# Kernel tuning notes

Hardware: AMD Instinct MI355X
Metric: run time of the kernel (lower is better)

Reference implementation:

```python
import jax, jax.numpy as jnp
import numpy as np

N_NODES = 100000
N_EDGES = 1600000
EPS = 1e-5


def _xavier(key, shape):
    fan_out, fan_in = shape
    lim = float(np.sqrt(6.0 / (fan_in + fan_out)))
    return jax.random.uniform(key, shape, jnp.float32, -lim, lim)


def setup_inputs() -> dict:
    key = jax.random.key(0)
    ks = jax.random.split(key, 16)
    d_in, d1, d2, d3 = 32, 64, 128, 64
    inp = {
        "x": jax.random.normal(ks[0], (N_NODES, d_in), jnp.float32),
        "edge_index": jax.random.randint(ks[1], (2, N_EDGES), 0, N_NODES, jnp.int64),
        "edge_weight": jax.random.uniform(ks[2], (N_EDGES,), jnp.float32),
        # GraphConv params: lin_rel (with bias) applied to aggregated msgs, lin_root (no bias)
        "W1_rel": _xavier(ks[3], (d1, d_in)), "b1": jnp.zeros((d1,), jnp.float32), "W1_root": _xavier(ks[4], (d1, d_in)),
        "W2_rel": _xavier(ks[5], (d2, d1)), "b2": jnp.zeros((d2,), jnp.float32), "W2_root": _xavier(ks[6], (d2, d1)),
        "W3_rel": _xavier(ks[7], (d3, d2)), "b3": jnp.zeros((d3,), jnp.float32), "W3_root": _xavier(ks[8], (d3, d2)),
        # BatchNorm affine params
        "g1": jnp.ones((d1,), jnp.float32), "be1": jnp.zeros((d1,), jnp.float32),
        "g2": jnp.ones((d2,), jnp.float32), "be2": jnp.zeros((d2,), jnp.float32),
        "g3": jnp.ones((d3,), jnp.float32), "be3": jnp.zeros((d3,), jnp.float32),
        # node-level classifier: Linear(64,32) -> ReLU -> Linear(32,2)
        "Wc1": _xavier(ks[9], (32, d3)), "bc1": jnp.zeros((32,), jnp.float32),
        "Wc2": _xavier(ks[10], (2, 32)), "bc2": jnp.zeros((2,), jnp.float32),
    }
    return inp


def _graph_conv(x, src, dst, W_rel, b, W_root, ew=None):
    msg = x[src]                      # [E, d] gather
    if ew is not None:
        msg = msg * ew[:, None]
    agg = jax.ops.segment_sum(msg, dst, num_segments=N_NODES)  # [N, d] scatter-add
    return agg @ W_rel.T + b + x @ W_root.T


def _bn(h, g, beta):
    mu = jnp.mean(h, axis=0)
    var = jnp.var(h, axis=0)
    return (h - mu) * jax.lax.rsqrt(var + EPS) * g + beta


def reference(x, edge_index, edge_weight,
              W1_rel, b1, W1_root, W2_rel, b2, W2_root, W3_rel, b3, W3_root,
              g1, be1, g2, be2, g3, be3, Wc1, bc1, Wc2, bc2):
    src, dst = edge_index[0], edge_index[1]
    h1 = jax.nn.relu(_bn(_graph_conv(x, src, dst, W1_rel, b1, W1_root), g1, be1))
    h2 = jax.nn.relu(_bn(_graph_conv(h1, src, dst, W2_rel, b2, W2_root), g2, be2))
    h3 = _bn(_graph_conv(h2, src, dst, W3_rel, b3, W3_root, edge_weight), g3, be3)
    h3 = jax.nn.relu(h3 + h1)  # residual (dims match, no projection)
    logits = jax.nn.relu(h3 @ Wc1.T + bc1) @ Wc2.T + bc2  # [N, 2]
    return logits
```

## Files before the change

### kernel.cpp

```cpp
#include <hip/hip_runtime.h>

#define N_NODES 100000
#define N_EDGES 1600000
#define EPSV 1e-5f

__device__ __forceinline__ ushort f2bf(float f) {
  unsigned u = __float_as_uint(f);
  unsigned r = (u + 0x7FFFu + ((u >> 16) & 1u)) >> 16;
  return (ushort)r;
}


__global__ void hist_kernel(const int* __restrict__ ei, int* __restrict__ cnt) {
  int e = blockIdx.x * blockDim.x + threadIdx.x;
  if (e >= N_EDGES) return;
  atomicAdd(&cnt[ei[N_EDGES + e]], 1);
}

#define SCAN_BLK 1024
#define SCAN_NB ((N_NODES + SCAN_BLK - 1) / SCAN_BLK)

__global__ void scan_phase1(const int* __restrict__ cnt, int* __restrict__ blocksum) {
  __shared__ int part[256];
  int base = blockIdx.x * SCAN_BLK + threadIdx.x * 4;
  int s = 0;
#pragma unroll
  for (int i = 0; i < 4; ++i) {
    int idx = base + i;
    if (idx < N_NODES) s += cnt[idx];
  }
  part[threadIdx.x] = s;
  __syncthreads();
  for (int d = 128; d > 0; d >>= 1) {
    if (threadIdx.x < d) part[threadIdx.x] += part[threadIdx.x + d];
    __syncthreads();
  }
  if (threadIdx.x == 0) blocksum[blockIdx.x] = part[0];
}

__global__ void scan_phase2(int* __restrict__ blocksum, int* __restrict__ rowptr) {
  __shared__ int part[128];
  int tid = threadIdx.x;
  int v = (tid < SCAN_NB) ? blocksum[tid] : 0;
  part[tid] = v;
  __syncthreads();
  for (int d = 1; d < 128; d <<= 1) {
    int t = (tid >= d) ? part[tid - d] : 0;
    __syncthreads();
    part[tid] += t;
    __syncthreads();
  }
  if (tid < SCAN_NB) blocksum[tid] = part[tid] - v;
  if (tid == 127) rowptr[N_NODES] = part[127];
}

__global__ void scan_phase3(const int* __restrict__ cnt, const int* __restrict__ blocksum,
                            int* __restrict__ rowptr, int* __restrict__ cursor) {
  __shared__ int part[256];
  int base = blockIdx.x * SCAN_BLK + threadIdx.x * 4;
  int c[4];
  int s = 0;
#pragma unroll
  for (int i = 0; i < 4; ++i) {
    int idx = base + i;
    c[i] = (idx < N_NODES) ? cnt[idx] : 0;
    s += c[i];
  }
  part[threadIdx.x] = s;
  __syncthreads();
  int me = s;
  for (int d = 1; d < 256; d <<= 1) {
    int t = (threadIdx.x >= d) ? part[threadIdx.x - d] : 0;
    __syncthreads();
    part[threadIdx.x] += t;
    __syncthreads();
  }
  int off = blocksum[blockIdx.x] + part[threadIdx.x] - me;
#pragma unroll
  for (int i = 0; i < 4; ++i) {
    int idx = base + i;
    if (idx < N_NODES) {
      rowptr[idx] = off;
      cursor[idx] = off;
      off += c[i];
    }
  }
}

#define FILL_SUB 256

__global__ void fill_kernel(const int* __restrict__ ei, const float* __restrict__ ew,
                            int* __restrict__ cursor, unsigned* __restrict__ col) {
  const int g = blockIdx.x & 7;
  const int sub = blockIdx.x >> 3;
  const int lo = g * 12500;
  const int hi = lo + 12500;
  const int EPB = (N_EDGES + FILL_SUB - 1) / FILL_SUB;
  const int beg = sub * EPB;
  const int end = min(beg + EPB, N_EDGES);
  for (int e = beg + (int)threadIdx.x; e < end; e += (int)blockDim.x) {
    int d = ei[N_EDGES + e];
    if (d < lo || d >= hi) continue;
    int p = atomicAdd(&cursor[d], 1);
    col[p] = ((unsigned)f2bf(ew[e]) << 17) | (unsigned)ei[e];
  }
}


__global__ void cast_bf16(const float* __restrict__ in, ushort* __restrict__ out, int n4) {
  int i = blockIdx.x * blockDim.x + threadIdx.x;
  if (i >= n4) return;
  float4 v = reinterpret_cast<const float4*>(in)[i];
  ushort4 o = make_ushort4(f2bf(v.x), f2bf(v.y), f2bf(v.z), f2bf(v.w));
  reinterpret_cast<ushort4*>(out)[i] = o;
}


#define SRC_OF(v) ((v) & 0x1FFFFu)
#define W_OF(v) __uint_as_float(((v) >> 17) << 16)

__global__ void gather_d32_bf(const ushort* __restrict__ xb, const int* __restrict__ rowptr,
                              const unsigned* __restrict__ col, float* __restrict__ agg) {
  int gid = blockIdx.x * blockDim.x + threadIdx.x;
  int n = gid >> 2;
  if (n >= N_NODES) return;
  int c = gid & 3;
  int beg = rowptr[n], end = rowptr[n + 1];
  float acc[8];
#pragma unroll
  for (int i = 0; i < 8; ++i) acc[i] = 0.f;
  int p = beg;
  for (; p + 1 < end; p += 2) {
    unsigned e0 = col[p], e1 = col[p + 1];
    uint4 u0 = *reinterpret_cast<const uint4*>(xb + (size_t)SRC_OF(e0) * 32 + c * 8);
    uint4 u1 = *reinterpret_cast<const uint4*>(xb + (size_t)SRC_OF(e1) * 32 + c * 8);
    unsigned a0[4] = {u0.x, u0.y, u0.z, u0.w};
    unsigned a1[4] = {u1.x, u1.y, u1.z, u1.w};
#pragma unroll
    for (int i = 0; i < 4; ++i) {
      acc[2 * i]     += __uint_as_float(a0[i] << 16) + __uint_as_float(a1[i] << 16);
      acc[2 * i + 1] += __uint_as_float(a0[i] & 0xFFFF0000u) +
                        __uint_as_float(a1[i] & 0xFFFF0000u);
    }
  }
  if (p < end) {
    unsigned e0 = col[p];
    uint4 u0 = *reinterpret_cast<const uint4*>(xb + (size_t)SRC_OF(e0) * 32 + c * 8);
    unsigned a0[4] = {u0.x, u0.y, u0.z, u0.w};
#pragma unroll
    for (int i = 0; i < 4; ++i) {
      acc[2 * i]     += __uint_as_float(a0[i] << 16);
      acc[2 * i + 1] += __uint_as_float(a0[i] & 0xFFFF0000u);
    }
  }
  float* op = agg + (size_t)n * 32 + c * 8;
  *reinterpret_cast<float4*>(op)     = make_float4(acc[0], acc[1], acc[2], acc[3]);
  *reinterpret_cast<float4*>(op + 4) = make_float4(acc[4], acc[5], acc[6], acc[7]);
}

template <bool WEIGHTED, bool TRANS>
__global__ void gather_d64_bf(const ushort* __restrict__ hb, const int* __restrict__ rowptr,
                              const unsigned* __restrict__ col,
                              const float* __restrict__ sc, const float* __restrict__ sh,
                              float* __restrict__ agg) {
  int gid = blockIdx.x * blockDim.x + threadIdx.x;
  int n = gid >> 3;
  if (n >= N_NODES) return;
  int c = gid & 7;
  int beg = rowptr[n], end = rowptr[n + 1];
  float sc8[8], sh8[8];
  if (TRANS) {
#pragma unroll
    for (int i = 0; i < 8; ++i) {
      sc8[i] = sc[c * 8 + i];
      sh8[i] = sh[c * 8 + i];
    }
  }
  float acc[8];
#pragma unroll
  for (int i = 0; i < 8; ++i) acc[i] = 0.f;

  auto body = [&](unsigned ev, const uint4& u) {
    float w = WEIGHTED ? W_OF(ev) : 1.f;
    unsigned uu[4] = {u.x, u.y, u.z, u.w};
#pragma unroll
    for (int i = 0; i < 4; ++i) {
      float lo = __uint_as_float(uu[i] << 16);
      float hi = __uint_as_float(uu[i] & 0xFFFF0000u);
      if (TRANS) {
        lo = fmaxf(fmaf(lo, sc8[2 * i], sh8[2 * i]), 0.f);
        hi = fmaxf(fmaf(hi, sc8[2 * i + 1], sh8[2 * i + 1]), 0.f);
      }
      if (WEIGHTED) {
        acc[2 * i]     = fmaf(lo, w, acc[2 * i]);
        acc[2 * i + 1] = fmaf(hi, w, acc[2 * i + 1]);
      } else {
        acc[2 * i]     += lo;
        acc[2 * i + 1] += hi;
      }
    }
  };

  int p = beg;
  for (; p + 1 < end; p += 2) {
    unsigned e0 = col[p], e1 = col[p + 1];
    uint4 u0 = *reinterpret_cast<const uint4*>(hb + (size_t)SRC_OF(e0) * 64 + c * 8);
    uint4 u1 = *reinterpret_cast<const uint4*>(hb + (size_t)SRC_OF(e1) * 64 + c * 8);
    body(e0, u0);
    body(e1, u1);
  }
  if (p < end) {
    unsigned e0 = col[p];
    uint4 u0 = *reinterpret_cast<const uint4*>(hb + (size_t)SRC_OF(e0) * 64 + c * 8);
    body(e0, u0);
  }
  float* op = agg + (size_t)n * 64 + c * 8;
  *reinterpret_cast<float4*>(op)     = make_float4(acc[0], acc[1], acc[2], acc[3]);
  *reinterpret_cast<float4*>(op + 4) = make_float4(acc[4], acc[5], acc[6], acc[7]);
}


template <int K1, int K2, int DO, int TA1, int TA2, int RADD, int STATS, int OUTM>
__global__ __launch_bounds__(256) void gemm_node(
    const float* __restrict__ A1, const float* __restrict__ A2,
    const float* __restrict__ W1, const float* __restrict__ W2,
    const float* __restrict__ sc, const float* __restrict__ sh,
    const float* __restrict__ R, float* __restrict__ out, ushort* __restrict__ outb,
    float* h2act, float* __restrict__ sums) {
  constexpr int K = K1 + K2;
  constexpr int NC = K / 64;
  constexpr int NJB = DO / 64;
  __shared__ __align__(16) float A_lds[64][68];
  __shared__ __align__(16) float W_lds[64][DO + 4];

  const int tid = threadIdx.x;
  const int tx = tid & 15, ty = tid >> 4;
  const int nbase = blockIdx.x * 64;

  float4 acc[4][NJB];
#pragma unroll
  for (int i = 0; i < 4; ++i)
#pragma unroll
    for (int jb = 0; jb < NJB; ++jb) acc[i][jb] = make_float4(0.f, 0.f, 0.f, 0.f);

#pragma unroll 1
  for (int c = 0; c < NC; ++c) {
    const int kb = c * 64;
    if (c) __syncthreads();
#pragma unroll
    for (int it = 0; it < 4; ++it) {
      int idx = it * 256 + tid;
      int nl = idx >> 4;
      int kq = (idx & 15) * 4;
      int k = kb + kq;
      int ng = nbase + nl;
      float4 v = make_float4(0.f, 0.f, 0.f, 0.f);
      bool isA1 = (K2 == 0) || (k < K1);
      if (ng < N_NODES) {
        if (isA1)
          v = *reinterpret_cast<const float4*>(A1 + (size_t)ng * K1 + k);
        else
          v = *reinterpret_cast<const float4*>(A2 + (size_t)ng * K2 + (k - K1));
      }
      if constexpr (TA1) {
        if (isA1) {
          float4 s4 = *reinterpret_cast<const float4*>(sc + k);
          float4 h4 = *reinterpret_cast<const float4*>(sh + k);
          v.x = fmaxf(fmaf(v.x, s4.x, h4.x), 0.f);
          v.y = fmaxf(fmaf(v.y, s4.y, h4.y), 0.f);
          v.z = fmaxf(fmaf(v.z, s4.z, h4.z), 0.f);
          v.w = fmaxf(fmaf(v.w, s4.w, h4.w), 0.f);
          if (ng < N_NODES)
            *reinterpret_cast<float4*>(h2act + (size_t)ng * K1 + k) = v;
        }
      }
      if constexpr (TA2 && K2 > 0) {
        if (!isA1) {
          float4 s4 = *reinterpret_cast<const float4*>(sc + (k - K1));
          float4 h4 = *reinterpret_cast<const float4*>(sh + (k - K1));
          v.x = fmaxf(fmaf(v.x, s4.x, h4.x), 0.f);
          v.y = fmaxf(fmaf(v.y, s4.y, h4.y), 0.f);
          v.z = fmaxf(fmaf(v.z, s4.z, h4.z), 0.f);
          v.w = fmaxf(fmaf(v.w, s4.w, h4.w), 0.f);
        }
      }
      *reinterpret_cast<float4*>(&A_lds[nl][kq]) = v;
    }
#pragma unroll
    for (int it = 0; it < DO / 4; ++it) {
      int idx = it * 256 + tid;
      int j = idx >> 6;
      int kl = idx & 63;
      int k = kb + kl;
      float w;
      if (K2 == 0 || k < K1) w = W1[(size_t)j * K1 + k];
      else w = W2[(size_t)j * K2 + (k - K1)];
      W_lds[kl][j] = w;
    }
    __syncthreads();
#pragma unroll 4
    for (int k4 = 0; k4 < 16; ++k4) {
      float4 a[4];
#pragma unroll
      for (int i = 0; i < 4; ++i)
        a[i] = *reinterpret_cast<const float4*>(&A_lds[ty * 4 + i][k4 * 4]);
#pragma unroll
      for (int q = 0; q < 4; ++q) {
#pragma unroll
        for (int jb = 0; jb < NJB; ++jb) {
          float4 w = *reinterpret_cast<const float4*>(&W_lds[k4 * 4 + q][jb * 64 + tx * 4]);
#pragma unroll
          for (int i = 0; i < 4; ++i) {
            float av = reinterpret_cast<const float*>(&a[i])[q];
            acc[i][jb].x = fmaf(av, w.x, acc[i][jb].x);
            acc[i][jb].y = fmaf(av, w.y, acc[i][jb].y);
            acc[i][jb].z = fmaf(av, w.z, acc[i][jb].z);
            acc[i][jb].w = fmaf(av, w.w, acc[i][jb].w);
          }
        }
      }
    }
  }
#pragma unroll
  for (int i = 0; i < 4; ++i) {
    int ng = nbase + ty * 4 + i;
    if (ng >= N_NODES) continue;
#pragma unroll
    for (int jb = 0; jb < NJB; ++jb) {
      if constexpr (RADD) {
        float4 rr = *reinterpret_cast<const float4*>(R + (size_t)ng * DO + jb * 64 + tx * 4);
        acc[i][jb].x += rr.x; acc[i][jb].y += rr.y;
        acc[i][jb].z += rr.z; acc[i][jb].w += rr.w;
      }
      size_t off = (size_t)ng * DO + jb * 64 + tx * 4;
      if constexpr (OUTM == 1) {
        ushort4 o = make_ushort4(f2bf(acc[i][jb].x), f2bf(acc[i][jb].y),
                                 f2bf(acc[i][jb].z), f2bf(acc[i][jb].w));
        *reinterpret_cast<ushort4*>((ushort*)out + off) = o;
      } else {
        *reinterpret_cast<float4*>(out + off) = acc[i][jb];
        if constexpr (OUTM == 2) {
          ushort4 o = make_ushort4(f2bf(acc[i][jb].x), f2bf(acc[i][jb].y),
                                   f2bf(acc[i][jb].z), f2bf(acc[i][jb].w));
          *reinterpret_cast<ushort4*>(outb + off) = o;
        }
      }
    }
  }
  if constexpr (STATS) {
    __syncthreads();
    float* sums_l = &A_lds[0][0];
    float* sq_l = &W_lds[0][0];
#pragma unroll
    for (int jb = 0; jb < NJB; ++jb) {
      float4 s = make_float4(0.f, 0.f, 0.f, 0.f);
      float4 q = make_float4(0.f, 0.f, 0.f, 0.f);
#pragma unroll
      for (int i = 0; i < 4; ++i) {
        if (nbase + ty * 4 + i < N_NODES) {
          float4 v = acc[i][jb];
          s.x += v.x; s.y += v.y; s.z += v.z; s.w += v.w;
          q.x = fmaf(v.x, v.x, q.x); q.y = fmaf(v.y, v.y, q.y);
          q.z = fmaf(v.z, v.z, q.z); q.w = fmaf(v.w, v.w, q.w);
        }
      }
      *reinterpret_cast<float4*>(&sums_l[ty * DO + jb * 64 + tx * 4]) = s;
      *reinterpret_cast<float4*>(&sq_l[ty * DO + jb * 64 + tx * 4]) = q;
    }
    __syncthreads();
    if (tid < DO) {
      float s = 0.f, q = 0.f;
#pragma unroll
      for (int t = 0; t < 16; ++t) {
        s += sums_l[t * DO + tid];
        q += sq_l[t * DO + tid];
      }
      unsafeAtomicAdd(&sums[tid], s);
      unsafeAtomicAdd(&sums[DO + tid], q);
    }
  }
}


__global__ void bn_finalize(const float* __restrict__ sums, const float* __restrict__ g,
                            const float* __restrict__ be, float* __restrict__ sc,
                            float* __restrict__ sh, int D) {
  int j = threadIdx.x;
  if (j >= D) return;
  const float invN = 1.f / (float)N_NODES;
  float mean = sums[j] * invN;
  float var = sums[D + j] * invN - mean * mean;
  float r = rsqrtf(var + EPSV);
  float scale = g[j] * r;
  sc[j] = scale;
  sh[j] = be[j] - mean * scale;
}


__global__ __launch_bounds__(256) void final_fused(
    const float* __restrict__ h3p, const float* __restrict__ h1p,
    const float* __restrict__ sc1, const float* __restrict__ sh1,
    const float* __restrict__ sc3, const float* __restrict__ sh3,
    const float* __restrict__ Wc1, const float* __restrict__ bc1,
    const float* __restrict__ Wc2, const float* __restrict__ bc2,
    float* __restrict__ out) {
  __shared__ __align__(16) float t_lds[64][68];
  __shared__ __align__(16) float w1_lds[64][36];
  __shared__ __align__(16) float c_lds[64][36];
  __shared__ __align__(16) float w2_lds[64];
  __shared__ __align__(16) float b1_lds[32];
  __shared__ float b2_lds[2];
  const int tid = threadIdx.x;
  const int nbase = blockIdx.x * 64;

#pragma unroll
  for (int it = 0; it < 4; ++it) {
    int idx = it * 256 + tid;
    int nl = idx >> 4;
    int k = (idx & 15) * 4;
    int ng = nbase + nl;
    float4 v = make_float4(0.f, 0.f, 0.f, 0.f);
    if (ng < N_NODES) {
      float4 p = *reinterpret_cast<const float4*>(h3p + (size_t)ng * 64 + k);
      float4 u = *reinterpret_cast<const float4*>(h1p + (size_t)ng * 64 + k);
      float4 sa = *reinterpret_cast<const float4*>(sc1 + k);
      float4 ha = *reinterpret_cast<const float4*>(sh1 + k);
      float4 sb = *reinterpret_cast<const float4*>(sc3 + k);
      float4 hb = *reinterpret_cast<const float4*>(sh3 + k);
      float h1x = fmaxf(fmaf(u.x, sa.x, ha.x), 0.f);
      float h1y = fmaxf(fmaf(u.y, sa.y, ha.y), 0.f);
      float h1z = fmaxf(fmaf(u.z, sa.z, ha.z), 0.f);
      float h1w = fmaxf(fmaf(u.w, sa.w, ha.w), 0.f);
      v.x = fmaxf(fmaf(p.x, sb.x, hb.x) + h1x, 0.f);
      v.y = fmaxf(fmaf(p.y, sb.y, hb.y) + h1y, 0.f);
      v.z = fmaxf(fmaf(p.z, sb.z, hb.z) + h1z, 0.f);
      v.w = fmaxf(fmaf(p.w, sb.w, hb.w) + h1w, 0.f);
    }
    *reinterpret_cast<float4*>(&t_lds[nl][k]) = v;
  }
#pragma unroll
  for (int it = 0; it < 8; ++it) {
    int idx = it * 256 + tid;
    int j = idx >> 6;
    int k = idx & 63;
    w1_lds[k][j] = Wc1[(size_t)j * 64 + k];
  }
  if (tid < 64) w2_lds[tid] = Wc2[tid];
  else if (tid < 96) b1_lds[tid - 64] = bc1[tid - 64];
  else if (tid < 98) b2_lds[tid - 96] = bc2[tid - 96];
  __syncthreads();

  {
    const int tx = tid & 7, ty = tid >> 3;
    float4 a0c = make_float4(0.f, 0.f, 0.f, 0.f);
    float4 a1c = make_float4(0.f, 0.f, 0.f, 0.f);
#pragma unroll 4
    for (int k4 = 0; k4 < 16; ++k4) {
      float4 a0 = *reinterpret_cast<const float4*>(&t_lds[ty * 2 + 0][k4 * 4]);
      float4 a1 = *reinterpret_cast<const float4*>(&t_lds[ty * 2 + 1][k4 * 4]);
#pragma unroll
      for (int q = 0; q < 4; ++q) {
        float4 w = *reinterpret_cast<const float4*>(&w1_lds[k4 * 4 + q][tx * 4]);
        float a0q = reinterpret_cast<const float*>(&a0)[q];
        float a1q = reinterpret_cast<const float*>(&a1)[q];
        a0c.x = fmaf(a0q, w.x, a0c.x); a0c.y = fmaf(a0q, w.y, a0c.y);
        a0c.z = fmaf(a0q, w.z, a0c.z); a0c.w = fmaf(a0q, w.w, a0c.w);
        a1c.x = fmaf(a1q, w.x, a1c.x); a1c.y = fmaf(a1q, w.y, a1c.y);
        a1c.z = fmaf(a1q, w.z, a1c.z); a1c.w = fmaf(a1q, w.w, a1c.w);
      }
    }
    float4 b = *reinterpret_cast<const float4*>(&b1_lds[tx * 4]);
    a0c.x = fmaxf(a0c.x + b.x, 0.f); a0c.y = fmaxf(a0c.y + b.y, 0.f);
    a0c.z = fmaxf(a0c.z + b.z, 0.f); a0c.w = fmaxf(a0c.w + b.w, 0.f);
    a1c.x = fmaxf(a1c.x + b.x, 0.f); a1c.y = fmaxf(a1c.y + b.y, 0.f);
    a1c.z = fmaxf(a1c.z + b.z, 0.f); a1c.w = fmaxf(a1c.w + b.w, 0.f);
    *reinterpret_cast<float4*>(&c_lds[ty * 2 + 0][tx * 4]) = a0c;
    *reinterpret_cast<float4*>(&c_lds[ty * 2 + 1][tx * 4]) = a1c;
  }
  __syncthreads();

  if (tid < 128) {
    int nl = tid >> 1, o = tid & 1;
    int ng = nbase + nl;
    if (ng < N_NODES) {
      float s = b2_lds[o];
#pragma unroll
      for (int k = 0; k < 32; ++k) s = fmaf(c_lds[nl][k], w2_lds[o * 32 + k], s);
      out[(size_t)ng * 2 + o] = s;
    }
  }
}


extern "C" void kernel_launch(void* const* d_in, const int* in_sizes, int n_in,
                              void* d_out, int out_size, void* d_ws, size_t ws_size,
                              hipStream_t stream) {
  const float* x      = (const float*)d_in[0];
  const int*   ei     = (const int*)d_in[1];
  const float* ew     = (const float*)d_in[2];
  const float* W1rel  = (const float*)d_in[3];
  const float* W1root = (const float*)d_in[5];
  const float* W2rel  = (const float*)d_in[6];
  const float* W2root = (const float*)d_in[8];
  const float* W3rel  = (const float*)d_in[9];
  const float* W3root = (const float*)d_in[11];
  const float* g1  = (const float*)d_in[12];
  const float* be1 = (const float*)d_in[13];
  const float* g2  = (const float*)d_in[14];
  const float* be2 = (const float*)d_in[15];
  const float* g3  = (const float*)d_in[16];
  const float* be3 = (const float*)d_in[17];
  const float* Wc1 = (const float*)d_in[18];
  const float* bc1 = (const float*)d_in[19];
  const float* Wc2 = (const float*)d_in[20];
  const float* bc2 = (const float*)d_in[21];

  float* ws = (float*)d_ws;
  const size_t NF = (size_t)N_NODES * 64;
  float* A = ws;
  float* B = ws + NF;
  float* C = ws + 2 * NF;
  float* E = ws + 3 * NF;
  float* X = ws + 5 * NF;
  float* S = X;
  int* rowptr   = (int*)(X + 1024);
  int* cnt      = rowptr + (N_NODES + 2);
  int* cursor   = cnt + N_NODES;
  int* blocksum = cursor + N_NODES;
  unsigned* col = (unsigned*)(blocksum + 128);

  ushort* xb     = (ushort*)B;
  ushort* h1preb = (ushort*)E;
  ushort* y2b    = (ushort*)B;

  hipMemsetAsync(S, 0, 1024 * sizeof(float), stream);
  hipMemsetAsync(cnt, 0, N_NODES * sizeof(int), stream);

  const int edgeBlocks = (N_EDGES + 255) / 256;
  const int tileBlocks = (N_NODES + 63) / 64;

  cast_bf16<<<(N_NODES * 32 / 4 + 255) / 256, 256, 0, stream>>>(x, xb, N_NODES * 32 / 4);

  hist_kernel<<<edgeBlocks, 256, 0, stream>>>(ei, cnt);
  scan_phase1<<<SCAN_NB, 256, 0, stream>>>(cnt, blocksum);
  scan_phase2<<<1, 128, 0, stream>>>(blocksum, rowptr);
  scan_phase3<<<SCAN_NB, 256, 0, stream>>>(cnt, blocksum, rowptr, cursor);
  fill_kernel<<<8 * FILL_SUB, 256, 0, stream>>>(ei, ew, cursor, col);

  gather_d32_bf<<<(N_NODES * 4 + 255) / 256, 256, 0, stream>>>(xb, rowptr, col, A);
  gemm_node<32, 32, 64, 0, 0, 0, 1, 2><<<tileBlocks, 256, 0, stream>>>(
      A, x, W1rel, W1root, nullptr, nullptr, nullptr, C, h1preb, nullptr, S);
  bn_finalize<<<1, 128, 0, stream>>>(S, g1, be1, S + 128, S + 192, 64);

  gather_d64_bf<false, true><<<(N_NODES * 8 + 255) / 256, 256, 0, stream>>>(
      h1preb, rowptr, col, S + 128, S + 192, A);
  gemm_node<64, 64, 128, 0, 1, 0, 1, 0><<<tileBlocks, 256, 0, stream>>>(
      A, C, W2rel, W2root, S + 128, S + 192, nullptr, E, nullptr, nullptr, S + 256);
  bn_finalize<<<1, 128, 0, stream>>>(S + 256, g2, be2, S + 512, S + 640, 128);

  gemm_node<128, 0, 64, 1, 0, 0, 0, 1><<<tileBlocks, 256, 0, stream>>>(
      E, nullptr, W3rel, nullptr, S + 512, S + 640, nullptr, (float*)y2b, nullptr, E, nullptr);

  gather_d64_bf<true, false><<<(N_NODES * 8 + 255) / 256, 256, 0, stream>>>(
      y2b, rowptr, col, nullptr, nullptr, A);
  gemm_node<128, 0, 64, 0, 0, 1, 1, 0><<<tileBlocks, 256, 0, stream>>>(
      E, nullptr, W3root, nullptr, nullptr, nullptr, A, B, nullptr, nullptr, S + 768);
  bn_finalize<<<1, 128, 0, stream>>>(S + 768, g3, be3, S + 896, S + 960, 64);

  final_fused<<<tileBlocks, 256, 0, stream>>>(B, C, S + 128, S + 192, S + 896, S + 960,
                                              Wc1, bc1, Wc2, bc2, (float*)d_out);
}
```

Baseline: 530.0 us.

## Pre-transpose GEMM weights once and halve K-chunk to shrink LDS footprint

Adds a one-shot kernel that transposes and concatenates all rel/root weight matrices into a K-major buffer. The node GEMM then copies weight tiles with coalesced float4 loads instead of strided scalar gathers, and processes K in 32-wide chunks, which roughly halves LDS per block. It also sets launch_bounds to a minimum of 4 blocks per CU. Higher occupancy and cheaper weight staging are traded for twice as many chunk iterations and barriers, plus one extra small kernel launch.

```diff
diff --git a/kernel.cpp b/kernel.cpp
--- a/kernel.cpp
+++ b/kernel.cpp
@@ -116,6 +116,33 @@
 }
 
 
+__global__ void wtrans_kernel(const float* __restrict__ W1rel, const float* __restrict__ W1root,
+                              const float* __restrict__ W2rel, const float* __restrict__ W2root,
+                              const float* __restrict__ W3rel, const float* __restrict__ W3root,
+                              float* __restrict__ Wt) {
+  int i = blockIdx.x * blockDim.x + threadIdx.x;
+  if (i >= 36864) return;
+  float v;
+  if (i < 4096) {
+    int k = i >> 6, j = i & 63;
+    v = (k < 32) ? W1rel[j * 32 + k] : W1root[j * 32 + (k - 32)];
+  } else if (i < 20480) {
+    int r = i - 4096;
+    int k = r >> 7, j = r & 127;
+    v = (k < 64) ? W2rel[j * 64 + k] : W2root[j * 64 + (k - 64)];
+  } else if (i < 28672) {
+    int r = i - 20480;
+    int k = r >> 6, j = r & 63;
+    v = W3rel[j * 128 + k];
+  } else {
+    int r = i - 28672;
+    int k = r >> 6, j = r & 63;
+    v = W3root[j * 128 + k];
+  }
+  Wt[i] = v;
+}
+
+
 #define SRC_OF(v) ((v) & 0x1FFFFu)
 #define W_OF(v) __uint_as_float(((v) >> 17) << 16)
 
@@ -221,17 +248,17 @@
 
 
 template <int K1, int K2, int DO, int TA1, int TA2, int RADD, int STATS, int OUTM>
-__global__ __launch_bounds__(256) void gemm_node(
+__global__ __launch_bounds__(256, 4) void gemm_node(
     const float* __restrict__ A1, const float* __restrict__ A2,
-    const float* __restrict__ W1, const float* __restrict__ W2,
+    const float* __restrict__ Wt,
     const float* __restrict__ sc, const float* __restrict__ sh,
     const float* __restrict__ R, float* __restrict__ out, ushort* __restrict__ outb,
     float* h2act, float* __restrict__ sums) {
   constexpr int K = K1 + K2;
-  constexpr int NC = K / 64;
+  constexpr int NC = K / 32;
   constexpr int NJB = DO / 64;
-  __shared__ __align__(16) float A_lds[64][68];
-  __shared__ __align__(16) float W_lds[64][DO + 4];
+  __shared__ __align__(16) float A_lds[64][36];
+  __shared__ __align__(16) float W_lds[32][DO];
 
   const int tid = threadIdx.x;
   const int tx = tid & 15, ty = tid >> 4;
@@ -245,13 +272,13 @@
 
 #pragma unroll 1
   for (int c = 0; c < NC; ++c) {
-    const int kb = c * 64;
+    const int kb = c * 32;
     if (c) __syncthreads();
 #pragma unroll
-    for (int it = 0; it < 4; ++it) {
+    for (int it = 0; it < 2; ++it) {
       int idx = it * 256 + tid;
-      int nl = idx >> 4;
-      int kq = (idx & 15) * 4;
+      int nl = idx >> 3;
+      int kq = (idx & 7) * 4;
       int k = kb + kq;
       int ng = nbase + nl;
       float4 v = make_float4(0.f, 0.f, 0.f, 0.f);
@@ -286,20 +313,16 @@
       }
       *reinterpret_cast<float4*>(&A_lds[nl][kq]) = v;
     }
-#pragma unroll
-    for (int it = 0; it < DO / 4; ++it) {
-      int idx = it * 256 + tid;
-      int j = idx >> 6;
-      int kl = idx & 63;
-      int k = kb + kl;
-      float w;
-      if (K2 == 0 || k < K1) w = W1[(size_t)j * K1 + k];
-      else w = W2[(size_t)j * K2 + (k - K1)];
-      W_lds[kl][j] = w;
-    }
-    __syncthreads();
-#pragma unroll 4
-    for (int k4 = 0; k4 < 16; ++k4) {
+    {
+      const float4* wsrc = reinterpret_cast<const float4*>(Wt + (size_t)kb * DO);
+      float4* wdst = reinterpret_cast<float4*>(&W_lds[0][0]);
+#pragma unroll
+      for (int it = 0; it < DO / 32; ++it)
+        wdst[it * 256 + tid] = wsrc[it * 256 + tid];
+    }
+    __syncthreads();
+#pragma unroll 2
+    for (int k4 = 0; k4 < 8; ++k4) {
       float4 a[4];
 #pragma unroll
       for (int i = 0; i < 4; ++i)
@@ -528,6 +551,11 @@
   int* cursor   = cnt + N_NODES;
   int* blocksum = cursor + N_NODES;
   unsigned* col = (unsigned*)(blocksum + 128);
+  float* Wt     = (float*)(col + N_EDGES);
+  float* Wt1  = Wt;
+  float* Wt2  = Wt + 4096;
+  float* Wt3r = Wt + 20480;
+  float* Wt3o = Wt + 28672;
 
   ushort* xb     = (ushort*)B;
   ushort* h1preb = (ushort*)E;
@@ -540,6 +568,7 @@
   const int tileBlocks = (N_NODES + 63) / 64;
 
   cast_bf16<<<(N_NODES * 32 / 4 + 255) / 256, 256, 0, stream>>>(x, xb, N_NODES * 32 / 4);
+  wtrans_kernel<<<144, 256, 0, stream>>>(W1rel, W1root, W2rel, W2root, W3rel, W3root, Wt);
 
   hist_kernel<<<edgeBlocks, 256, 0, stream>>>(ei, cnt);
   scan_phase1<<<SCAN_NB, 256, 0, stream>>>(cnt, blocksum);
@@ -549,22 +578,22 @@
 
   gather_d32_bf<<<(N_NODES * 4 + 255) / 256, 256, 0, stream>>>(xb, rowptr, col, A);
   gemm_node<32, 32, 64, 0, 0, 0, 1, 2><<<tileBlocks, 256, 0, stream>>>(
-      A, x, W1rel, W1root, nullptr, nullptr, nullptr, C, h1preb, nullptr, S);
+      A, x, Wt1, nullptr, nullptr, nullptr, C, h1preb, nullptr, S);
   bn_finalize<<<1, 128, 0, stream>>>(S, g1, be1, S + 128, S + 192, 64);
 
   gather_d64_bf<false, true><<<(N_NODES * 8 + 255) / 256, 256, 0, stream>>>(
       h1preb, rowptr, col, S + 128, S + 192, A);
   gemm_node<64, 64, 128, 0, 1, 0, 1, 0><<<tileBlocks, 256, 0, stream>>>(
-      A, C, W2rel, W2root, S + 128, S + 192, nullptr, E, nullptr, nullptr, S + 256);
+      A, C, Wt2, S + 128, S + 192, nullptr, E, nullptr, nullptr, S + 256);
   bn_finalize<<<1, 128, 0, stream>>>(S + 256, g2, be2, S + 512, S + 640, 128);
 
   gemm_node<128, 0, 64, 1, 0, 0, 0, 1><<<tileBlocks, 256, 0, stream>>>(
-      E, nullptr, W3rel, nullptr, S + 512, S + 640, nullptr, (float*)y2b, nullptr, E, nullptr);
+      E, nullptr, Wt3r, S + 512, S + 640, nullptr, (float*)y2b, nullptr, E, nullptr);
 
   gather_d64_bf<true, false><<<(N_NODES * 8 + 255) / 256, 256, 0, stream>>>(
       y2b, rowptr, col, nullptr, nullptr, A);
   gemm_node<128, 0, 64, 0, 0, 1, 1, 0><<<tileBlocks, 256, 0, stream>>>(
-      E, nullptr, W3root, nullptr, nullptr, nullptr, A, B, nullptr, nullptr, S + 768);
+      E, nullptr, Wt3o, nullptr, nullptr, A, B, nullptr, nullptr, S + 768);
   bn_finalize<<<1, 128, 0, stream>>>(S + 768, g3, be3, S + 896, S + 960, 64);
 
   final_fused<<<tileBlocks, 256, 0, stream>>>(B, C, S + 128, S + 192, S + 896, S + 960,
```

New measurement: 479.7 us. 1.1x faster.
